# Kernel optimization log

Hardware: AMD Instinct MI355X
Metric: run time of the kernel (lower is better)

## Reference

```python
import jax, jax.numpy as jnp
import numpy as np

N_NODES = 10000
N_EDGES = 640000
D_FEAT = 128
D_OUT = 128


def setup_inputs() -> dict:
    key = jax.random.key(0)
    k1, k2, k3, k4, k5 = jax.random.split(key, 5)
    h = jax.random.normal(k1, (N_NODES, D_FEAT), dtype=jnp.float32)
    norm = jax.random.uniform(k2, (N_NODES, 1), dtype=jnp.float32)
    # glorot-style scale for the dense weight (4*in_feats -> out_feats)
    weight = jax.random.normal(k3, (4 * D_FEAT, D_OUT), dtype=jnp.float32) * (2.0 / (4 * D_FEAT + D_OUT)) ** 0.5
    src = jax.random.randint(k4, (N_EDGES,), 0, N_NODES, dtype=jnp.int32)
    dst = jax.random.randint(k5, (N_EDGES,), 0, N_NODES, dtype=jnp.int32)
    return {"h": h, "norm": norm, "weight": weight, "src": src, "dst": dst}


def reference(h, norm, weight, src, dst):
    N = h.shape[0]
    # tf.math.l2_normalize: x * rsqrt(max(sum(x^2), 1e-12))
    h = h * jax.lax.rsqrt(jnp.maximum(jnp.sum(h * h, axis=-1, keepdims=True), 1e-12))
    h = h * norm  # [N, F]

    m = h[src]  # edge messages [E, F] (shared gather)

    # pass 1: copy_src + sum -> agg_h, then * norm
    agg_h = jax.ops.segment_sum(m, dst, num_segments=N) * norm

    # pass 2: mailbox max and mean(hard_sigmoid) over incoming messages
    deg = jax.ops.segment_sum(jnp.ones((m.shape[0],), dtype=h.dtype), dst, num_segments=N)  # [N]
    mx = jax.ops.segment_max(m, dst, num_segments=N)
    mx = jnp.where(deg[:, None] > 0, mx, 0.0)  # nodes w/o in-edges keep zeros
    # keras hard_sigmoid: clip(0.2*x + 0.5, 0, 1)
    hs_sum = jax.ops.segment_sum(jnp.clip(0.2 * m + 0.5, 0.0, 1.0), dst, num_segments=N)
    mean_hs = hs_sum / jnp.maximum(deg, 1.0)[:, None]
    accum_h = jnp.concatenate((mx, mean_hs), axis=1) * norm  # [N, 2F]

    out = jnp.concatenate((h, agg_h, accum_h), axis=1) @ weight  # [N, 4F] @ [4F, D_OUT]
    return jax.nn.relu(out)
```

## Files before the change

kernel.cpp:

```cpp
#include <hip/hip_runtime.h>
#include <math.h>

#define DF 128
#define DK 512
#define DO 128
#define CAP 128
#define CSTR 32

typedef __attribute__((ext_vector_type(8))) short bf16x8;
typedef __attribute__((ext_vector_type(8))) unsigned short u16x8;
typedef __attribute__((ext_vector_type(4))) float f32x4;

__device__ inline unsigned short f2bf(float x) {
    unsigned int u = __builtin_bit_cast(unsigned int, x);
    unsigned int r = (u + 0x7FFFu + ((u >> 16) & 1u)) >> 16;
    return (unsigned short)r;
}
__device__ inline float bf2f(unsigned short b) {
    unsigned int u = ((unsigned int)b) << 16;
    return __builtin_bit_cast(float, u);
}

__global__ void pb_k(const float* __restrict__ W, unsigned short* __restrict__ Wt,
                     const float* __restrict__ h, const float* __restrict__ norm,
                     unsigned short* __restrict__ Xb, int* __restrict__ cur,
                     unsigned short* __restrict__ bsrc,
                     const int* __restrict__ src, const int* __restrict__ dst,
                     int N, int E, int nbE, int nbN) {
    int b = blockIdx.x;
    if (b < nbE) {
        int t  = b * 256 + threadIdx.x;
        int e0 = t * 4;
        if (e0 + 3 < E) {
            const int4 d4 = *reinterpret_cast<const int4*>(dst + e0);
            const int4 s4 = *reinterpret_cast<const int4*>(src + e0);
            int p0 = atomicAdd(&cur[(size_t)d4.x * CSTR], 1);
            int p1 = atomicAdd(&cur[(size_t)d4.y * CSTR], 1);
            int p2 = atomicAdd(&cur[(size_t)d4.z * CSTR], 1);
            int p3 = atomicAdd(&cur[(size_t)d4.w * CSTR], 1);
            if (p0 < CAP) bsrc[((size_t)d4.x << 7) + p0] = (unsigned short)s4.x;
            if (p1 < CAP) bsrc[((size_t)d4.y << 7) + p1] = (unsigned short)s4.y;
            if (p2 < CAP) bsrc[((size_t)d4.z << 7) + p2] = (unsigned short)s4.z;
            if (p3 < CAP) bsrc[((size_t)d4.w << 7) + p3] = (unsigned short)s4.w;
        } else {
            for (int e = e0; e < E; ++e) {
                int d = dst[e];
                int p = atomicAdd(&cur[(size_t)d * CSTR], 1);
                if (p < CAP) bsrc[((size_t)d << 7) + p] = (unsigned short)src[e];
            }
        }
    } else if (b < nbE + nbN) {
        int wid = threadIdx.x >> 6;
        int t   = threadIdx.x & 63;
        int n   = (b - nbE) * 4 + wid;
        if (n >= N) return;
        const float2 hv = reinterpret_cast<const float2*>(h + (size_t)n * DF)[t];
        float ss = hv.x * hv.x + hv.y * hv.y;
        #pragma unroll
        for (int o = 32; o > 0; o >>= 1) ss += __shfl_xor(ss, o);
        float scale = rsqrtf(fmaxf(ss, 1e-12f)) * norm[n];
        ushort2 o2;
        o2.x = f2bf(hv.x * scale);
        o2.y = f2bf(hv.y * scale);
        reinterpret_cast<ushort2*>(Xb + (size_t)n * DK)[t] = o2;
    } else {
        int t = (b - nbE - nbN) * 256 + threadIdx.x;
        int c  = t >> 6;
        int k0 = (t & 63) * 8;
        u16x8 v;
        #pragma unroll
        for (int j = 0; j < 8; ++j) v[j] = f2bf(W[(size_t)(k0 + j) * DO + c]);
        *reinterpret_cast<u16x8*>(Wt + (size_t)c * DK + k0) = v;
    }
}

__global__ void __launch_bounds__(512, 8) fused_k(const unsigned short* __restrict__ Xb,
                                                  const unsigned short* __restrict__ Wt,
                                                  const int* __restrict__ cur,
                                                  const float* __restrict__ norm,
                                                  const unsigned short* __restrict__ bsrc,
                                                  float* __restrict__ out, int N) {
    __shared__ unsigned short Xs[16][520];
    __shared__ unsigned short sid[8][128];
    int tid = threadIdx.x;
    int w = tid >> 6;
    int l = tid & 63;
    int nb0 = blockIdx.x * 8;
    int n = nb0 + w;
    int rq = l >> 4;
    int lc = l & 15;
    bool valid = (n < N);

    int cntt = valid ? cur[(size_t)n * CSTR] : 0;
    int cnt  = min(cntt, CAP);

    if (valid) {
        reinterpret_cast<unsigned int*>(&sid[w][0])[l] =
            reinterpret_cast<const unsigned int*>(bsrc + ((size_t)n << 7))[l];
        if (l < 16)
            *reinterpret_cast<u16x8*>(&Xs[w][lc * 8]) =
                *reinterpret_cast<const u16x8*>(Xb + (size_t)n * DK + lc * 8);
    }

    float s[8] = {0.f, 0.f, 0.f, 0.f, 0.f, 0.f, 0.f, 0.f};
    float m[8] = {-INFINITY, -INFINITY, -INFINITY, -INFINITY,
                  -INFINITY, -INFINITY, -INFINITY, -INFINITY};
    #pragma unroll 8
    for (int j = rq; j < cnt; j += 4) {
        int sj = (int)sid[w][j];
        bf16x8 v = *reinterpret_cast<const bf16x8*>(Xb + ((size_t)sj << 9) + lc * 8);
        #pragma unroll
        for (int f = 0; f < 8; ++f) {
            float a = bf2f((unsigned short)v[f]);
            s[f] += a;
            m[f] = fmaxf(m[f], a);
        }
    }
    #pragma unroll
    for (int f = 0; f < 8; ++f) {
        s[f] += __shfl_xor(s[f], 16);
        s[f] += __shfl_xor(s[f], 32);
        m[f] = fmaxf(m[f], __shfl_xor(m[f], 16));
        m[f] = fmaxf(m[f], __shfl_xor(m[f], 32));
    }
    if (valid && l < 16) {
        float nm  = norm[n];
        float inv = 1.0f / fmaxf((float)cntt, 1.0f);
        u16x8 o1, o2, o3;
        #pragma unroll
        for (int f = 0; f < 8; ++f) {
            o1[f] = f2bf(s[f] * nm);
            float mm = (cnt > 0) ? m[f] : 0.0f;
            o2[f] = f2bf(mm * nm);
            o3[f] = f2bf((0.2f * s[f] + 0.5f * (float)cnt) * inv * nm);
        }
        *reinterpret_cast<u16x8*>(&Xs[w][128 + lc * 8]) = o1;
        *reinterpret_cast<u16x8*>(&Xs[w][256 + lc * 8]) = o2;
        *reinterpret_cast<u16x8*>(&Xs[w][384 + lc * 8]) = o3;
    }
    __syncthreads();

    int r  = l & 15;
    int kg = l >> 4;
    f32x4 acc = {};
    const unsigned short* B = Wt + (size_t)(w * 16 + r) * DK;
    #pragma unroll
    for (int ks = 0; ks < 16; ++ks) {
        bf16x8 a = *reinterpret_cast<const bf16x8*>(&Xs[r][ks * 32 + kg * 8]);
        bf16x8 b = *reinterpret_cast<const bf16x8*>(B + ks * 32 + kg * 8);
        acc = __builtin_amdgcn_mfma_f32_16x16x32_bf16(a, b, acc, 0, 0, 0);
    }
    if (kg < 2) {
        #pragma unroll
        for (int q = 0; q < 4; ++q) {
            int rr = nb0 + kg * 4 + q;
            if (rr < N) out[(size_t)rr * DO + w * 16 + r] = fmaxf(acc[q], 0.0f);
        }
    }
}

extern "C" void kernel_launch(void* const* d_in, const int* in_sizes, int n_in,
                              void* d_out, int out_size, void* d_ws, size_t ws_size,
                              hipStream_t stream) {
    const float* h    = (const float*)d_in[0];
    const float* norm = (const float*)d_in[1];
    const float* W    = (const float*)d_in[2];
    const int*   src  = (const int*)d_in[3];
    const int*   dst  = (const int*)d_in[4];
    float* out = (float*)d_out;

    int N = in_sizes[0] / DF;
    int E = in_sizes[3];

    unsigned short* Xb = (unsigned short*)d_ws;
    unsigned short* Wt = Xb + (size_t)N * DK;
    int* cur = (int*)(Wt + (size_t)DO * DK);
    unsigned short* bsrc = (unsigned short*)(cur + (size_t)N * CSTR);

    int nbE = (E / 4 + 255) / 256;
    int nbN = (N + 3) / 4;

    hipMemsetAsync(cur, 0, (size_t)N * CSTR * sizeof(int), stream);
    pb_k   <<<dim3(nbE + nbN + 32), dim3(256), 0, stream>>>(W, Wt, h, norm, Xb, cur, bsrc,
                                                            src, dst, N, E, nbE, nbN);
    fused_k<<<dim3((N + 7) / 8),    dim3(512), 0, stream>>>(Xb, Wt, cur, norm, bsrc, out, N);
}
```

Measured before the change: 75.66 us.

## Replace memset with in-kernel counter zeroing, split bucketing kernel, pack bf16 accumulate

The separate hipMemsetAsync of the strided counter array is removed; prep_k now zeroes each node's counter while it normalizes h, and edge bucketing moves into its own kernel launched afterwards. The gather loop unpacks bf16 pairs with shifts and masks into float2 vectors so the compiler can use packed add and max. Launch bounds on fused_k drop from 8 to 6 waves per unit to give it more registers. This trades one memset for an extra kernel launch, and the bucketing no longer overlaps with the normalization work.

```diff
diff --git a/kernel.cpp b/kernel.cpp
--- a/kernel.cpp
+++ b/kernel.cpp
@@ -10,50 +10,32 @@
 typedef __attribute__((ext_vector_type(8))) short bf16x8;
 typedef __attribute__((ext_vector_type(8))) unsigned short u16x8;
 typedef __attribute__((ext_vector_type(4))) float f32x4;
+typedef __attribute__((ext_vector_type(2))) float f32x2;
 
 __device__ inline unsigned short f2bf(float x) {
     unsigned int u = __builtin_bit_cast(unsigned int, x);
     unsigned int r = (u + 0x7FFFu + ((u >> 16) & 1u)) >> 16;
     return (unsigned short)r;
 }
-__device__ inline float bf2f(unsigned short b) {
-    unsigned int u = ((unsigned int)b) << 16;
-    return __builtin_bit_cast(float, u);
-}
 
-__global__ void pb_k(const float* __restrict__ W, unsigned short* __restrict__ Wt,
-                     const float* __restrict__ h, const float* __restrict__ norm,
-                     unsigned short* __restrict__ Xb, int* __restrict__ cur,
-                     unsigned short* __restrict__ bsrc,
-                     const int* __restrict__ src, const int* __restrict__ dst,
-                     int N, int E, int nbE, int nbN) {
+__global__ void prep_k(const float* __restrict__ W, unsigned short* __restrict__ Wt,
+                       const float* __restrict__ h, const float* __restrict__ norm,
+                       unsigned short* __restrict__ Xb, int* __restrict__ cur, int N) {
     int b = blockIdx.x;
-    if (b < nbE) {
-        int t  = b * 256 + threadIdx.x;
-        int e0 = t * 4;
-        if (e0 + 3 < E) {
-            const int4 d4 = *reinterpret_cast<const int4*>(dst + e0);
-            const int4 s4 = *reinterpret_cast<const int4*>(src + e0);
-            int p0 = atomicAdd(&cur[(size_t)d4.x * CSTR], 1);
-            int p1 = atomicAdd(&cur[(size_t)d4.y * CSTR], 1);
-            int p2 = atomicAdd(&cur[(size_t)d4.z * CSTR], 1);
-            int p3 = atomicAdd(&cur[(size_t)d4.w * CSTR], 1);
-            if (p0 < CAP) bsrc[((size_t)d4.x << 7) + p0] = (unsigned short)s4.x;
-            if (p1 < CAP) bsrc[((size_t)d4.y << 7) + p1] = (unsigned short)s4.y;
-            if (p2 < CAP) bsrc[((size_t)d4.z << 7) + p2] = (unsigned short)s4.z;
-            if (p3 < CAP) bsrc[((size_t)d4.w << 7) + p3] = (unsigned short)s4.w;
-        } else {
-            for (int e = e0; e < E; ++e) {
-                int d = dst[e];
-                int p = atomicAdd(&cur[(size_t)d * CSTR], 1);
-                if (p < CAP) bsrc[((size_t)d << 7) + p] = (unsigned short)src[e];
-            }
-        }
-    } else if (b < nbE + nbN) {
+    if (b < 32) {
+        int t = b * 256 + threadIdx.x;
+        int c  = t >> 6;
+        int k0 = (t & 63) * 8;
+        u16x8 v;
+        #pragma unroll
+        for (int j = 0; j < 8; ++j) v[j] = f2bf(W[(size_t)(k0 + j) * DO + c]);
+        *reinterpret_cast<u16x8*>(Wt + (size_t)c * DK + k0) = v;
+    } else {
         int wid = threadIdx.x >> 6;
         int t   = threadIdx.x & 63;
-        int n   = (b - nbE) * 4 + wid;
+        int n   = (b - 32) * 4 + wid;
         if (n >= N) return;
+        if (t == 0) cur[(size_t)n * CSTR] = 0;
         const float2 hv = reinterpret_cast<const float2*>(h + (size_t)n * DF)[t];
         float ss = hv.x * hv.x + hv.y * hv.y;
         #pragma unroll
@@ -63,18 +45,34 @@
         o2.x = f2bf(hv.x * scale);
         o2.y = f2bf(hv.y * scale);
         reinterpret_cast<ushort2*>(Xb + (size_t)n * DK)[t] = o2;
-    } else {
-        int t = (b - nbE - nbN) * 256 + threadIdx.x;
-        int c  = t >> 6;
-        int k0 = (t & 63) * 8;
-        u16x8 v;
-        #pragma unroll
-        for (int j = 0; j < 8; ++j) v[j] = f2bf(W[(size_t)(k0 + j) * DO + c]);
-        *reinterpret_cast<u16x8*>(Wt + (size_t)c * DK + k0) = v;
     }
 }
 
-__global__ void __launch_bounds__(512, 8) fused_k(const unsigned short* __restrict__ Xb,
+__global__ void bucket_k(const int* __restrict__ src, const int* __restrict__ dst,
+                         int* __restrict__ cur, unsigned short* __restrict__ bsrc, int E) {
+    int t  = blockIdx.x * blockDim.x + threadIdx.x;
+    int e0 = t * 4;
+    if (e0 + 3 < E) {
+        const int4 d4 = *reinterpret_cast<const int4*>(dst + e0);
+        const int4 s4 = *reinterpret_cast<const int4*>(src + e0);
+        int p0 = atomicAdd(&cur[(size_t)d4.x * CSTR], 1);
+        int p1 = atomicAdd(&cur[(size_t)d4.y * CSTR], 1);
+        int p2 = atomicAdd(&cur[(size_t)d4.z * CSTR], 1);
+        int p3 = atomicAdd(&cur[(size_t)d4.w * CSTR], 1);
+        if (p0 < CAP) bsrc[((size_t)d4.x << 7) + p0] = (unsigned short)s4.x;
+        if (p1 < CAP) bsrc[((size_t)d4.y << 7) + p1] = (unsigned short)s4.y;
+        if (p2 < CAP) bsrc[((size_t)d4.z << 7) + p2] = (unsigned short)s4.z;
+        if (p3 < CAP) bsrc[((size_t)d4.w << 7) + p3] = (unsigned short)s4.w;
+    } else {
+        for (int e = e0; e < E; ++e) {
+            int d = dst[e];
+            int p = atomicAdd(&cur[(size_t)d * CSTR], 1);
+            if (p < CAP) bsrc[((size_t)d << 7) + p] = (unsigned short)src[e];
+        }
+    }
+}
+
+__global__ void __launch_bounds__(512, 6) fused_k(const unsigned short* __restrict__ Xb,
                                                   const unsigned short* __restrict__ Wt,
                                                   const int* __restrict__ cur,
                                                   const float* __restrict__ norm,
@@ -102,19 +100,32 @@
                 *reinterpret_cast<const u16x8*>(Xb + (size_t)n * DK + lc * 8);
     }
 
-    float s[8] = {0.f, 0.f, 0.f, 0.f, 0.f, 0.f, 0.f, 0.f};
-    float m[8] = {-INFINITY, -INFINITY, -INFINITY, -INFINITY,
-                  -INFINITY, -INFINITY, -INFINITY, -INFINITY};
+    f32x2 s2[4], m2[4];
+    #pragma unroll
+    for (int q = 0; q < 4; ++q) {
+        s2[q] = f32x2{0.0f, 0.0f};
+        m2[q] = f32x2{-INFINITY, -INFINITY};
+    }
     #pragma unroll 8
     for (int j = rq; j < cnt; j += 4) {
         int sj = (int)sid[w][j];
-        bf16x8 v = *reinterpret_cast<const bf16x8*>(Xb + ((size_t)sj << 9) + lc * 8);
+        uint4 v = *reinterpret_cast<const uint4*>(Xb + ((size_t)sj << 9) + lc * 8);
         #pragma unroll
-        for (int f = 0; f < 8; ++f) {
-            float a = bf2f((unsigned short)v[f]);
-            s[f] += a;
-            m[f] = fmaxf(m[f], a);
+        for (int q = 0; q < 4; ++q) {
+            unsigned int wv = (&v.x)[q];
+            f32x2 val;
+            val.x = __builtin_bit_cast(float, wv << 16);
+            val.y = __builtin_bit_cast(float, wv & 0xFFFF0000u);
+            s2[q] += val;
+            m2[q] = __builtin_elementwise_max(m2[q], val);
         }
+    }
+
+    float s[8], m[8];
+    #pragma unroll
+    for (int q = 0; q < 4; ++q) {
+        s[2 * q] = s2[q].x;  s[2 * q + 1] = s2[q].y;
+        m[2 * q] = m2[q].x;  m[2 * q + 1] = m2[q].y;
     }
     #pragma unroll
     for (int f = 0; f < 8; ++f) {
@@ -177,11 +188,8 @@
     int* cur = (int*)(Wt + (size_t)DO * DK);
     unsigned short* bsrc = (unsigned short*)(cur + (size_t)N * CSTR);
 
-    int nbE = (E / 4 + 255) / 256;
-    int nbN = (N + 3) / 4;
-
-    hipMemsetAsync(cur, 0, (size_t)N * CSTR * sizeof(int), stream);
-    pb_k   <<<dim3(nbE + nbN + 32), dim3(256), 0, stream>>>(W, Wt, h, norm, Xb, cur, bsrc,
-                                                            src, dst, N, E, nbE, nbN);
-    fused_k<<<dim3((N + 7) / 8),    dim3(512), 0, stream>>>(Xb, Wt, cur, norm, bsrc, out, N);
+    int nblk = (N + 3) / 4 + 32;
+    prep_k  <<<dim3(nblk),              dim3(256), 0, stream>>>(W, Wt, h, norm, Xb, cur, N);
+    bucket_k<<<dim3((E / 4 + 255)/256), dim3(256), 0, stream>>>(src, dst, cur, bsrc, E);
+    fused_k <<<dim3((N + 7) / 8),       dim3(512), 0, stream>>>(Xb, Wt, cur, norm, bsrc, out, N);
 }
```

After: 74.90 us. No clear change (-1.0%).
